# Optimization experiments

Hardware: AMD Instinct MI355X
Metric: run time of the kernel (lower is better)

Reference implementation:

```python
import jax, jax.numpy as jnp
import numpy as np

BS = 4  # block_size == stride (non-overlapping)
EPS = 1e-5

def _to_blocks(x):
    # (B,C,H,W) -> (B*Hb*Wb, C, BS*BS), matching nn.Unfold(k=BS, stride=BS)
    B, C, H, W = x.shape
    Hb, Wb = H // BS, W // BS
    x = x.reshape(B, C, Hb, BS, Wb, BS).transpose(0, 2, 4, 1, 3, 5)
    return x.reshape(B * Hb * Wb, C, BS * BS)

def _from_blocks(x, B, C, H, W):
    Hb, Wb = H // BS, W // BS
    x = x.reshape(B, Hb, Wb, C, BS, BS).transpose(0, 3, 1, 4, 2, 5)
    return x.reshape(B, C, H, W)


def setup_inputs() -> dict:
    key = jax.random.key(0)
    ks = jax.random.split(key, 8)
    B, C, H, W = 8, 64, 256, 256
    P = 64  # proj_dim
    s = 1.0 / np.sqrt(C)
    return {
        "query_x": jax.random.normal(ks[0], (B, C, H, W), jnp.float32),
        "ref_x": jax.random.normal(ks[1], (B, C, H, W), jnp.float32),
        "Wq": jax.random.normal(ks[2], (P, C), jnp.float32) * s,
        "Wk": jax.random.normal(ks[3], (P, C), jnp.float32) * s,
        "Wv": jax.random.normal(ks[4], (P, C), jnp.float32) * s,
        "Wfc": jax.random.normal(ks[5], (C, P), jnp.float32) * (1.0 / np.sqrt(P)),
        "gn_w": jnp.ones((C,), jnp.float32),
        "gn_b": jnp.zeros((C,), jnp.float32),
    }


def reference(query_x, ref_x, Wq, Wk, Wv, Wfc, gn_w, gn_b):
    B, C, H, W = query_x.shape
    qb = _to_blocks(query_x)   # (Nb, C, 16)
    rb = _to_blocks(ref_x)     # (Nb, C, 16)

    q = jnp.einsum('pc,bcn->bpn', Wq, qb)
    k = jnp.einsum('pc,bcn->bpn', Wk, rb)
    v = jnp.einsum('pc,bcn->bpn', Wv, rb)

    energy = jnp.einsum('bcn,bcm->bnm', q, k)          # (Nb, 16, 16)
    attn = jax.nn.softmax(energy, axis=-1)
    out = jnp.einsum('bcm,bnm->bcn', v, attn)          # (Nb, P, 16)

    x = jnp.einsum('cp,bpn->bcn', Wfc, out)            # (Nb, C, 16)

    # GroupNorm(num_groups=1) over (C, N) per block
    mu = jnp.mean(x, axis=(1, 2), keepdims=True)
    var = jnp.var(x, axis=(1, 2), keepdims=True)
    x = (x - mu) * jax.lax.rsqrt(var + EPS)
    x = x * gn_w[None, :, None] + gn_b[None, :, None]

    x = x + qb  # residual
    return _from_blocks(x, B, C, H, W)
```

## Files before the change

### kernel.cpp

```cpp
#include <hip/hip_runtime.h>
#include <cstdint>


typedef float  f4    __attribute__((ext_vector_type(4)));
typedef float  f32x4 __attribute__((ext_vector_type(4)));
typedef short  s16x4 __attribute__((ext_vector_type(4)));
typedef short  s16x8 __attribute__((ext_vector_type(8)));
typedef unsigned short u16;
typedef __bf16 bf16;

#define MFMA16(a,b,c) __builtin_amdgcn_mfma_f32_16x16x16bf16_1k((a),(b),(c),0,0,0)
#define MFMA32(a,b,c) __builtin_amdgcn_mfma_f32_16x16x32_bf16((a),(b),(c),0,0,0)

#define DPP_ROR(x, N)                                                         \
  __builtin_bit_cast(float, __builtin_amdgcn_mov_dpp(                         \
      __builtin_bit_cast(int, (x)), 0x120 + (N), 0xF, 0xF, 1))

__device__ __align__(16) u16 g_wpack[4 * 4096];

__device__ __forceinline__ u16 bfbits(float x) {
  return __builtin_bit_cast(u16, (bf16)x);
}

__device__ __forceinline__ void gload_lds16(const float* g, float* l) {
  __builtin_amdgcn_global_load_lds(
      (const __attribute__((address_space(1))) void*)g,
      (__attribute__((address_space(3))) void*)l, 16, 0, 0);
}

__global__ void prep_w(const float* __restrict__ Wq, const float* __restrict__ Wk,
                       const float* __restrict__ Wv, const float* __restrict__ Wfc)
{
  const int t = threadIdx.x;
  const float* Wm[3] = {Wq, Wk, Wv};
#pragma unroll
  for (int s = 0; s < 3; ++s) {
    const float* W = Wm[s];
    for (int e = t; e < 512; e += 256) {
      const int tile = e >> 6, l = e & 63;
      const int row = 16 * (tile >> 1) + (l & 15);
      const int col = 32 * (tile & 1) + 8 * (l >> 4);
#pragma unroll
      for (int j = 0; j < 8; ++j)
        g_wpack[s * 4096 + e * 8 + j] = bfbits(W[row * 64 + col + j]);
    }
  }
  for (int e = t; e < 1024; e += 256) {
    const int tile = e >> 6, l = e & 63;
    const int row = 16 * (tile >> 2) + (l & 15);
    const int col = 16 * (tile & 3) + 4 * (l >> 4);
#pragma unroll
    for (int j = 0; j < 4; ++j)
      g_wpack[3 * 4096 + e * 4 + j] = bfbits(Wfc[row * 64 + col + j]);
  }
}

__global__ void __launch_bounds__(256, 2)
cvbt14(const float* __restrict__ qx, const float* __restrict__ rx,
       const float* __restrict__ gw, const float* __restrict__ gb,
       float* __restrict__ out)
{
  __shared__ __align__(16) float sQ[2][4096];
  __shared__ u16   sP[4 * 320];
  __shared__ float sGn[128];

  const int tid  = threadIdx.x;
  const int wv   = tid >> 6, lane = tid & 63;
  const int n = lane & 15, g = lane >> 4, rp = n >> 2, wl = n & 3;

  if (tid < 128) sGn[tid] = (tid < 64) ? gw[tid] : gb[tid - 64];

  s16x8 Wq8[4][2], Wk8[4][2], Wv8[4][2];
  s16x4 Wf4[4][4];
#pragma unroll
  for (int a = 0; a < 4; ++a) {
#pragma unroll
    for (int c2 = 0; c2 < 2; ++c2) {
      Wq8[a][c2] = *(const s16x8*)(g_wpack + 0 * 4096 + ((a * 2 + c2) * 64 + lane) * 8);
      Wk8[a][c2] = *(const s16x8*)(g_wpack + 1 * 4096 + ((a * 2 + c2) * 64 + lane) * 8);
      Wv8[a][c2] = *(const s16x8*)(g_wpack + 2 * 4096 + ((a * 2 + c2) * 64 + lane) * 8);
    }
#pragma unroll
    for (int c4 = 0; c4 < 4; ++c4)
      Wf4[a][c4] = *(const s16x4*)(g_wpack + 3 * 4096 + ((a * 4 + c4) * 64 + lane) * 4);
  }

  uint32_t goff[4]; int lbase[4];
#pragma unroll
  for (int s = 0; s < 4; ++s) {
    const int j = s * 4 + wv;
    const int c = 4 * j + (lane >> 4);
    const int r = (lane >> 2) & 3, y = lane & 3;
    const int w4 = y ^ r ^ ((c >> 3) & 3);
    goff[s]  = (uint32_t)c * 65536u + (uint32_t)r * 256u + (uint32_t)w4 * 4u;
    lbase[s] = j * 256;
  }

  const int bid = blockIdx.x;
  const int wid = (bid & 7) * 128 + (bid >> 3);
  const int si0 = wid * 8;

  auto sbase = [](int si) -> uint32_t {
    return ((uint32_t)si >> 10) * 4194304u + (((uint32_t)si >> 4) & 63) * 1024u +
           ((uint32_t)si & 15) * 16u;
  };

  const uint32_t xro = (uint32_t)rp * 256u + (uint32_t)(4 * wv + wl);

  uint32_t sb = sbase(si0);
#pragma unroll
  for (int s = 0; s < 4; ++s) gload_lds16(qx + sb + goff[s], &sQ[0][lbase[s]]);
  asm volatile("s_waitcnt vmcnt(0) lgkmcnt(0)" ::: "memory");

  const f32x4 zero = {0.f, 0.f, 0.f, 0.f};
  u16* sPw = &sP[wv * 320];
  int pp = 0;

#pragma unroll 1
  for (int t = 0; t < 8; ++t) {
    const uint32_t nsb = sbase(si0 + (t < 7 ? t + 1 : t));

    asm volatile("s_waitcnt vmcnt(4)" ::: "memory");
    __builtin_amdgcn_s_barrier();
    __builtin_amdgcn_sched_barrier(0);

    float xr[2][8];
#pragma unroll
    for (int kt = 0; kt < 2; ++kt)
#pragma unroll
      for (int j = 0; j < 8; ++j)
        xr[kt][j] = rx[sb + xro + (uint32_t)(32 * kt + 8 * g + j) * 65536u];
    __builtin_amdgcn_sched_barrier(0);

    if (t < 7) {
#pragma unroll
      for (int s = 0; s < 4; ++s)
        gload_lds16(qx + nsb + goff[s], &sQ[pp ^ 1][lbase[s]]);
    }
    __builtin_amdgcn_sched_barrier(0);

    s16x8 fqh[2], fql[2];
#pragma unroll
    for (int kt = 0; kt < 2; ++kt)
#pragma unroll
      for (int j = 0; j < 8; ++j) {
        const int addr = (32 * kt + 8 * g + j) * 64 + rp * 16 + 4 * (wv ^ rp ^ g) + wl;
        float x1 = sQ[pp][addr];
        bf16 h = (bf16)x1;
        fqh[kt][j] = (short)__builtin_bit_cast(u16, h);
        fql[kt][j] = (short)bfbits(x1 - (float)h);
      }
    f32x4 aq[4];
#pragma unroll
    for (int mt = 0; mt < 4; ++mt) {
      aq[mt] = zero;
#pragma unroll
      for (int kt = 0; kt < 2; ++kt) {
        aq[mt] = MFMA32(Wq8[mt][kt], fqh[kt], aq[mt]);
        aq[mt] = MFMA32(Wq8[mt][kt], fql[kt], aq[mt]);
      }
    }

    s16x8 frh[2], frl[2];
#pragma unroll
    for (int kt = 0; kt < 2; ++kt)
#pragma unroll
      for (int j = 0; j < 8; ++j) {
        float x2 = xr[kt][j];
        bf16 h = (bf16)x2;
        frh[kt][j] = (short)__builtin_bit_cast(u16, h);
        frl[kt][j] = (short)bfbits(x2 - (float)h);
      }
    f32x4 ak[4], av[4];
#pragma unroll
    for (int mt = 0; mt < 4; ++mt) { ak[mt] = zero; av[mt] = zero; }
#pragma unroll
    for (int mt = 0; mt < 4; ++mt)
#pragma unroll
      for (int kt = 0; kt < 2; ++kt) {
        ak[mt] = MFMA32(Wk8[mt][kt], frh[kt], ak[mt]);
        ak[mt] = MFMA32(Wk8[mt][kt], frl[kt], ak[mt]);
      }
#pragma unroll
    for (int nt2 = 0; nt2 < 4; ++nt2)
#pragma unroll
      for (int kt = 0; kt < 2; ++kt)
        av[nt2] = MFMA32(frh[kt], Wv8[nt2][kt], av[nt2]);

    s16x4 qh[4], ql[4], kh[4], kl[4];
#pragma unroll
    for (int kt = 0; kt < 4; ++kt)
#pragma unroll
      for (int r = 0; r < 4; ++r) {
        bf16 h = (bf16)aq[kt][r];
        qh[kt][r] = (short)__builtin_bit_cast(u16, h);
        ql[kt][r] = (short)bfbits(aq[kt][r] - (float)h);
        bf16 h2 = (bf16)ak[kt][r];
        kh[kt][r] = (short)__builtin_bit_cast(u16, h2);
        kl[kt][r] = (short)bfbits(ak[kt][r] - (float)h2);
      }

    f32x4 e0 = zero, e1 = zero, e2 = zero;
#pragma unroll
    for (int kt = 0; kt < 4; ++kt) {
      e0 = MFMA16(qh[kt], kh[kt], e0);
      e1 = MFMA16(qh[kt], kl[kt], e1);
      e2 = MFMA16(ql[kt], kh[kt], e2);
    }
    f32x4 e;
#pragma unroll
    for (int r = 0; r < 4; ++r) e[r] = (e0[r] + e1[r]) + e2[r];

#pragma unroll
    for (int r = 0; r < 4; ++r) {
      float x = e[r];
      float m = x;
      m = fmaxf(m, DPP_ROR(m, 8));
      m = fmaxf(m, DPP_ROR(m, 4));
      m = fmaxf(m, DPP_ROR(m, 2));
      m = fmaxf(m, DPP_ROR(m, 1));
      float p = __expf(x - m);
      float s = p;
      s += DPP_ROR(s, 8);
      s += DPP_ROR(s, 4);
      s += DPP_ROR(s, 2);
      s += DPP_ROR(s, 1);
      sPw[(4 * g + r) * 20 + n] = bfbits(p * __builtin_amdgcn_rcpf(s));
    }

    s16x4 pa = *(const s16x4*)&sPw[n * 20 + 4 * g];
    f32x4 ao[4];
#pragma unroll
    for (int mt = 0; mt < 4; ++mt) {
      s16x4 vb;
#pragma unroll
      for (int j = 0; j < 4; ++j) vb[j] = (short)bfbits(av[mt][j]);
      ao[mt] = MFMA16(vb, pa, zero);
    }

    s16x4 ob[4];
#pragma unroll
    for (int kt = 0; kt < 4; ++kt)
#pragma unroll
      for (int j = 0; j < 4; ++j) ob[kt][j] = (short)bfbits(ao[kt][j]);
    f32x4 xa[4];
#pragma unroll
    for (int mt = 0; mt < 4; ++mt) {
      xa[mt] = zero;
#pragma unroll
      for (int kt = 0; kt < 4; ++kt)
        xa[mt] = MFMA16(Wf4[mt][kt], ob[kt], xa[mt]);
    }

    float s1 = 0.f, s2 = 0.f;
#pragma unroll
    for (int mt = 0; mt < 4; ++mt)
#pragma unroll
      for (int r = 0; r < 4; ++r) {
        float v = xa[mt][r];
        s1 += v; s2 += v * v;
      }
    s1 += DPP_ROR(s1, 8);  s2 += DPP_ROR(s2, 8);
    s1 += DPP_ROR(s1, 4);  s2 += DPP_ROR(s2, 4);
    s1 += DPP_ROR(s1, 2);  s2 += DPP_ROR(s2, 2);
    s1 += DPP_ROR(s1, 1);  s2 += DPP_ROR(s2, 1);
    s1 += __shfl_xor(s1, 16);  s2 += __shfl_xor(s2, 16);
    s1 += __shfl_xor(s1, 32);  s2 += __shfl_xor(s2, 32);
    const float mean = s1 * (1.f / 1024.f);
    const float var  = s2 * (1.f / 1024.f) - mean * mean;
    const float rstd = rsqrtf(var + 1e-5f);

#pragma unroll
    for (int mt = 0; mt < 4; ++mt)
#pragma unroll
      for (int r = 0; r < 4; ++r) {
        const int row = 16 * mt + 4 * g + r;
        const int addr = row * 64 + rp * 16 + 4 * (wv ^ rp ^ ((row >> 3) & 3)) + wl;
        sQ[pp][addr] = (xa[mt][r] - mean) * rstd * sGn[row] + sGn[64 + row] + sQ[pp][addr];
      }

    asm volatile("s_waitcnt lgkmcnt(0)" ::: "memory");
    __builtin_amdgcn_s_barrier();
    __builtin_amdgcn_sched_barrier(0);

#pragma unroll
    for (int s = 0; s < 4; ++s) {
      f4 o = *(const f4*)&sQ[pp][lbase[s] + lane * 4];
      __builtin_nontemporal_store(o, (f4*)(out + sb + goff[s]));
    }

    pp ^= 1;
    sb = nsb;
  }
}

extern "C" void kernel_launch(void* const* d_in, const int* in_sizes, int n_in,
                              void* d_out, int out_size, void* d_ws, size_t ws_size,
                              hipStream_t stream) {
  const float* qx  = (const float*)d_in[0];
  const float* rx  = (const float*)d_in[1];
  const float* Wq  = (const float*)d_in[2];
  const float* Wk  = (const float*)d_in[3];
  const float* Wv  = (const float*)d_in[4];
  const float* Wfc = (const float*)d_in[5];
  const float* gw  = (const float*)d_in[6];
  const float* gb  = (const float*)d_in[7];
  float* out = (float*)d_out;

  prep_w<<<dim3(1), dim3(256), 0, stream>>>(Wq, Wk, Wv, Wfc);
  cvbt14<<<dim3(1024), dim3(256), 0, stream>>>(qx, rx, gw, gb, out);
}
```

Measured before the change: 108.3 us.

## Prefetch ref_x into per-wave LDS and drop block-wide barriers

Reference-input loads move from direct per-iteration global reads into registers to asynchronous 4-byte global-to-LDS loads. They are double-issued one tile ahead, so their latency overlaps the current tile's compute. The query tile's LDS layout becomes per-wave private slices with padding, so each wave reads, writes back its residual output and stores without the two block-level barriers per iteration. The risk is correctness: the reused ref LDS buffer is overwritten by the prefetch while prior LDS reads may still be pending, and the code relies on vmcnt ordering. It also raises LDS usage.

```diff
diff --git a/kernel.cpp b/kernel.cpp
--- a/kernel.cpp
+++ b/kernel.cpp
@@ -27,6 +27,11 @@
       (const __attribute__((address_space(1))) void*)g,
       (__attribute__((address_space(3))) void*)l, 16, 0, 0);
 }
+__device__ __forceinline__ void gload_lds4(const float* g, float* l) {
+  __builtin_amdgcn_global_load_lds(
+      (const __attribute__((address_space(1))) void*)g,
+      (__attribute__((address_space(3))) void*)l, 4, 0, 0);
+}
 
 __global__ void prep_w(const float* __restrict__ Wq, const float* __restrict__ Wk,
                        const float* __restrict__ Wv, const float* __restrict__ Wfc)
@@ -56,11 +61,12 @@
 }
 
 __global__ void __launch_bounds__(256, 2)
-cvbt14(const float* __restrict__ qx, const float* __restrict__ rx,
+cvbt15(const float* __restrict__ qx, const float* __restrict__ rx,
        const float* __restrict__ gw, const float* __restrict__ gb,
        float* __restrict__ out)
 {
-  __shared__ __align__(16) float sQ[2][4096];
+  __shared__ __align__(16) float sQ[2][4][1056];
+  __shared__ __align__(16) float sXr[4][1024];
   __shared__ u16   sP[4 * 320];
   __shared__ float sGn[128];
 
@@ -69,6 +75,7 @@
   const int n = lane & 15, g = lane >> 4, rp = n >> 2, wl = n & 3;
 
   if (tid < 128) sGn[tid] = (tid < 64) ? gw[tid] : gb[tid - 64];
+  __syncthreads();
 
   s16x8 Wq8[4][2], Wk8[4][2], Wv8[4][2];
   s16x4 Wf4[4][4];
@@ -85,16 +92,13 @@
       Wf4[a][c4] = *(const s16x4*)(g_wpack + 3 * 4096 + ((a * 4 + c4) * 64 + lane) * 4);
   }
 
-  uint32_t goff[4]; int lbase[4];
-#pragma unroll
-  for (int s = 0; s < 4; ++s) {
-    const int j = s * 4 + wv;
-    const int c = 4 * j + (lane >> 4);
-    const int r = (lane >> 2) & 3, y = lane & 3;
-    const int w4 = y ^ r ^ ((c >> 3) & 3);
-    goff[s]  = (uint32_t)c * 65536u + (uint32_t)r * 256u + (uint32_t)w4 * 4u;
-    lbase[s] = j * 256;
-  }
+  const uint32_t vq = (uint32_t)(lane >> 2) * 65536u + (uint32_t)(lane & 3) * 256u;
+  const uint32_t vr = (uint32_t)g * 524288u + (uint32_t)rp * 256u + (uint32_t)wl;
+
+  float* xrb = &sXr[wv][0];
+  float* qA  = &sQ[0][wv][0];
+  float* qB  = &sQ[1][wv][0];
+  u16*   sPw = &sP[wv * 320];
 
   const int bid = blockIdx.x;
   const int wid = (bid & 7) * 128 + (bid >> 3);
@@ -104,38 +108,49 @@
     return ((uint32_t)si >> 10) * 4194304u + (((uint32_t)si >> 4) & 63) * 1024u +
            ((uint32_t)si & 15) * 16u;
   };
-
-  const uint32_t xro = (uint32_t)rp * 256u + (uint32_t)(4 * wv + wl);
+  const uint32_t wv4 = (uint32_t)wv * 4u;
 
   uint32_t sb = sbase(si0);
 #pragma unroll
-  for (int s = 0; s < 4; ++s) gload_lds16(qx + sb + goff[s], &sQ[0][lbase[s]]);
-  asm volatile("s_waitcnt vmcnt(0) lgkmcnt(0)" ::: "memory");
+  for (int m = 0; m < 16; ++m)
+    gload_lds4(rx + sb + wv4 + vr + (uint32_t)((m >> 3) * 32 + (m & 7)) * 65536u,
+               &xrb[m * 64]);
+#pragma unroll
+  for (int i = 0; i < 4; ++i)
+    gload_lds16(qx + sb + wv4 + vq + (uint32_t)i * 1048576u, &qA[i * 264]);
+  asm volatile("s_waitcnt vmcnt(0)" ::: "memory");
 
   const f32x4 zero = {0.f, 0.f, 0.f, 0.f};
-  u16* sPw = &sP[wv * 320];
-  int pp = 0;
 
 #pragma unroll 1
   for (int t = 0; t < 8; ++t) {
     const uint32_t nsb = sbase(si0 + (t < 7 ? t + 1 : t));
+    float* qc = (t & 1) ? qB : qA;
+    float* qn = (t & 1) ? qA : qB;
 
     asm volatile("s_waitcnt vmcnt(4)" ::: "memory");
-    __builtin_amdgcn_s_barrier();
     __builtin_amdgcn_sched_barrier(0);
 
-    float xr[2][8];
+    s16x8 frh[2], frl[2];
 #pragma unroll
     for (int kt = 0; kt < 2; ++kt)
 #pragma unroll
-      for (int j = 0; j < 8; ++j)
-        xr[kt][j] = rx[sb + xro + (uint32_t)(32 * kt + 8 * g + j) * 65536u];
+      for (int j = 0; j < 8; ++j) {
+        float x2 = xrb[(kt * 8 + j) * 64 + lane];
+        bf16 h = (bf16)x2;
+        frh[kt][j] = (short)__builtin_bit_cast(u16, h);
+        frl[kt][j] = (short)bfbits(x2 - (float)h);
+      }
     __builtin_amdgcn_sched_barrier(0);
 
     if (t < 7) {
 #pragma unroll
-      for (int s = 0; s < 4; ++s)
-        gload_lds16(qx + nsb + goff[s], &sQ[pp ^ 1][lbase[s]]);
+      for (int m = 0; m < 16; ++m)
+        gload_lds4(rx + nsb + wv4 + vr + (uint32_t)((m >> 3) * 32 + (m & 7)) * 65536u,
+                   &xrb[m * 64]);
+#pragma unroll
+      for (int i = 0; i < 4; ++i)
+        gload_lds16(qx + nsb + wv4 + vq + (uint32_t)i * 1048576u, &qn[i * 264]);
     }
     __builtin_amdgcn_sched_barrier(0);
 
@@ -144,8 +159,8 @@
     for (int kt = 0; kt < 2; ++kt)
 #pragma unroll
       for (int j = 0; j < 8; ++j) {
-        const int addr = (32 * kt + 8 * g + j) * 64 + rp * 16 + 4 * (wv ^ rp ^ g) + wl;
-        float x1 = sQ[pp][addr];
+        const int c = 32 * kt + 8 * g + j;
+        float x1 = qc[(c >> 4) * 264 + (c & 15) * 16 + n];
         bf16 h = (bf16)x1;
         fqh[kt][j] = (short)__builtin_bit_cast(u16, h);
         fql[kt][j] = (short)bfbits(x1 - (float)h);
@@ -161,16 +176,6 @@
       }
     }
 
-    s16x8 frh[2], frl[2];
-#pragma unroll
-    for (int kt = 0; kt < 2; ++kt)
-#pragma unroll
-      for (int j = 0; j < 8; ++j) {
-        float x2 = xr[kt][j];
-        bf16 h = (bf16)x2;
-        frh[kt][j] = (short)__builtin_bit_cast(u16, h);
-        frl[kt][j] = (short)bfbits(x2 - (float)h);
-      }
     f32x4 ak[4], av[4];
 #pragma unroll
     for (int mt = 0; mt < 4; ++mt) { ak[mt] = zero; av[mt] = zero; }
@@ -207,13 +212,10 @@
       e1 = MFMA16(qh[kt], kl[kt], e1);
       e2 = MFMA16(ql[kt], kh[kt], e2);
     }
-    f32x4 e;
-#pragma unroll
-    for (int r = 0; r < 4; ++r) e[r] = (e0[r] + e1[r]) + e2[r];
 
 #pragma unroll
     for (int r = 0; r < 4; ++r) {
-      float x = e[r];
+      float x = (e0[r] + e1[r]) + e2[r];
       float m = x;
       m = fmaxf(m, DPP_ROR(m, 8));
       m = fmaxf(m, DPP_ROR(m, 4));
@@ -275,21 +277,17 @@
 #pragma unroll
       for (int r = 0; r < 4; ++r) {
         const int row = 16 * mt + 4 * g + r;
-        const int addr = row * 64 + rp * 16 + 4 * (wv ^ rp ^ ((row >> 3) & 3)) + wl;
-        sQ[pp][addr] = (xa[mt][r] - mean) * rstd * sGn[row] + sGn[64 + row] + sQ[pp][addr];
-      }
-
-    asm volatile("s_waitcnt lgkmcnt(0)" ::: "memory");
-    __builtin_amdgcn_s_barrier();
-    __builtin_amdgcn_sched_barrier(0);
-
-#pragma unroll
-    for (int s = 0; s < 4; ++s) {
-      f4 o = *(const f4*)&sQ[pp][lbase[s] + lane * 4];
-      __builtin_nontemporal_store(o, (f4*)(out + sb + goff[s]));
-    }
-
-    pp ^= 1;
+        const int addr = mt * 264 + (4 * g + r) * 16 + n;
+        qc[addr] = (xa[mt][r] - mean) * rstd * sGn[row] + sGn[64 + row] + qc[addr];
+      }
+
+#pragma unroll
+    for (int i = 0; i < 4; ++i) {
+      f4 o = *(const f4*)&qc[i * 264 + lane * 4];
+      __builtin_nontemporal_store(
+          o, (f4*)(out + sb + wv4 + vq + (uint32_t)i * 1048576u));
+    }
+
     sb = nsb;
   }
 }
@@ -308,5 +306,5 @@
   float* out = (float*)d_out;
 
   prep_w<<<dim3(1), dim3(256), 0, stream>>>(Wq, Wk, Wv, Wfc);
-  cvbt14<<<dim3(1024), dim3(256), 0, stream>>>(qx, rx, gw, gb, out);
-}
+  cvbt15<<<dim3(1024), dim3(256), 0, stream>>>(qx, rx, gw, gb, out);
+}
```

Measured after the change: 432.2 us. 299% more time.
